# Kernel optimization log

Measured on AMD Instinct MI355X. Metric: run time of the kernel, lower is better.

## Reference

```python
import jax, jax.numpy as jnp
import numpy as np

B, C, H, W = 8, 1, 384, 384
INF2 = float(H * H + W * W + 1)  # 'infinite' squared distance


def _edt_single(feat):
    # Exact Euclidean distance transform: distance from every pixel to the
    # nearest True pixel in `feat` [H, W]. Separable squared-distance min.
    j = jnp.arange(W)
    dj2 = ((j[:, None] - j[None, :]).astype(jnp.float32)) ** 2  # [W, W']
    # g2[i, j] = min_{j': feat[i, j']} (j - j')^2
    g2 = jnp.min(jnp.where(feat[:, None, :], dj2[None, :, :], INF2), axis=2)  # [H, W]
    i = jnp.arange(H)
    di2 = ((i[:, None] - i[None, :]).astype(jnp.float32)) ** 2  # [H, H']
    # d2[i, j] = min_{i'} g2[i', j] + (i - i')^2
    d2 = jnp.min(di2[:, :, None] + g2[None, :, :], axis=1)  # [H, W]
    return jnp.sqrt(jnp.minimum(d2, INF2))


def _distance_map(target):
    # Signed distance map: EDT(1-m) - EDT(m), normalized by global max-abs,
    # matching BoundaryLoss._compute_distance_map (scipy distance_transform_edt).
    m = target.reshape(-1, H, W)

    def per_img(mi):
        fg = mi > 0.5
        pos = _edt_single(fg)        # dist to nearest foreground (EDT of 1-m)
        neg = _edt_single(~fg)       # dist to nearest background (EDT of m)
        return pos - neg

    dist = jax.lax.map(per_img, m).reshape(target.shape)
    maxabs = jnp.max(jnp.abs(dist))
    return jnp.where(maxabs > 0, dist / maxabs, dist)


def _lovasz_flat(logits, labels):
    # Binary Lovasz hinge on flat vectors (one sample).
    signs = 2.0 * labels - 1.0
    errors = 1.0 - logits * signs
    order = jnp.argsort(-errors)          # descending sort, perm is constant w.r.t. grads
    errors_sorted = errors[order]
    gt_sorted = labels[order]
    gts = jnp.sum(gt_sorted)
    intersection = gts - jnp.cumsum(gt_sorted)
    union = gts + jnp.cumsum(1.0 - gt_sorted)
    jaccard = 1.0 - intersection / (union + 1e-7)
    grad = jnp.concatenate([jaccard[:1], jaccard[1:] - jaccard[:-1]])
    return jnp.dot(jax.nn.relu(errors_sorted), grad)


def _combined_loss(pred, target):
    # BCE with logits (stable): max(x,0) - x*z + log1p(exp(-|x|)), mean.
    bce = jnp.mean(jnp.maximum(pred, 0.0) - pred * target + jnp.log1p(jnp.exp(-jnp.abs(pred))))
    # Dice.
    p = jax.nn.sigmoid(pred)
    smooth = 1.0
    intersection = jnp.sum(p * target)
    union = jnp.sum(p) + jnp.sum(target)
    dice = 1.0 - (2.0 * intersection + smooth) / (union + smooth)
    # Boundary: mean(sigmoid(pred) * signed_dist_map(target)); dist map is constant.
    dist_map = jax.lax.stop_gradient(_distance_map(target))
    boundary = jnp.mean(p * dist_map)
    # Lovasz hinge, per-sample over flattened pixels, then mean over batch.
    lovasz = jnp.mean(jax.vmap(_lovasz_flat)(pred.reshape(B, -1), target.reshape(B, -1)))
    loss = 0.3 * bce + 0.3 * dice + 0.2 * boundary + 0.2 * lovasz
    return jnp.clip(loss, 0.0, 100.0)


def setup_inputs() -> dict:
    key = jax.random.key(0)
    k1, k2 = jax.random.split(key)
    pred = jax.random.normal(k1, (B, C, H, W), dtype=jnp.float32)
    target = (jax.random.uniform(k2, (B, C, H, W)) < 0.3).astype(jnp.float32)
    return {"pred": pred, "target": target}


def reference(pred, target):
    return _combined_loss(pred, target)
```

## Files before the change

kernel.cpp:

```cpp
#include <hip/hip_runtime.h>
#include <hip/hip_bf16.h>
#include <math.h>

#define PSZ   147456
#define NTOT  1179648
#define WW    384
#define HH    384
#define NIMG  8
#define NBINH 2048
#define INF2F 294913.0f
#define GV2   1152
#define HPART 8

static __device__ __forceinline__ float errval(float x, float z) {
    float s = __fsub_rn(__fmul_rn(2.0f, z), 1.0f);
    return __fsub_rn(1.0f, __fmul_rn(x, s));
}
static __device__ __forceinline__ int binof(float e) {
    int b = (int)(__fmul_rn(e, 256.0f));
    return b > (NBINH - 1) ? (NBINH - 1) : b;
}
static __device__ __forceinline__ float d2f(int d) {
    return (float)(d * d);
}

struct DPair { int df, db; };
static __device__ __forceinline__ DPair ndist2(const unsigned long long* __restrict__ m, int p) {
    const int BIG = 1 << 20;
    int q = p >> 6, b = p & 63;
    int df = BIG, db = BIG;
    {
        unsigned long long w = m[q];
        unsigned long long tf = w >> b;
        unsigned long long tb = (~w) >> b;
        if (tf) df = __builtin_ctzll(tf);
        if (tb) db = __builtin_ctzll(tb);
        for (int u = q + 1; (df == BIG || db == BIG) && u < 6; ++u) {
            w = m[u];
            if (df == BIG && w)  df = u * 64 + __builtin_ctzll(w)  - p;
            if (db == BIG && ~w) db = u * 64 + __builtin_ctzll(~w) - p;
        }
    }
    {
        unsigned long long w = m[q];
        unsigned long long tf = w << (63 - b);
        unsigned long long tb = (~w) << (63 - b);
        int lf = BIG, lb = BIG;
        if (tf) lf = __builtin_clzll(tf);
        if (tb) lb = __builtin_clzll(tb);
        for (int u = q - 1; (lf == BIG || lb == BIG) && u >= 0; --u) {
            w = m[u];
            if (lf == BIG && w)  lf = p - (u * 64 + 63 - __builtin_clzll(w));
            if (lb == BIG && ~w) lb = p - (u * 64 + 63 - __builtin_clzll(~w));
        }
        if (lf < df) df = lf;
        if (lb < db) db = lb;
    }
    DPair r;
    r.df = (df > 600) ? 600 : df;
    r.db = (db > 600) ? 600 : db;
    return r;
}

__global__ __launch_bounds__(1024) void k_pre(const float* __restrict__ tgt,
                                              const float* __restrict__ pred,
                                              unsigned int* __restrict__ g2,
                                              unsigned long long* __restrict__ histp,
                                              unsigned int* __restrict__ maxabsBits,
                                              unsigned int* __restrict__ elect) {
    __shared__ unsigned long long h[NBINH * 2];
    for (int q = threadIdx.x; q < NBINH * 2; q += 1024) h[q] = 0ull;
    if (blockIdx.x == 0 && threadIdx.x == 0) { maxabsBits[0] = 0u; elect[0] = 0u; }
    __syncthreads();
    int img  = blockIdx.x & 7;
    int part = blockIdx.x >> 3;
    int wv = threadIdx.x >> 6, l = threadIdx.x & 63;
#pragma unroll
    for (int rr = 0; rr < 3; ++rr) {
        int row = img * HH + part * 48 + wv * 3 + rr;
        const float* tr = tgt  + (size_t)row * WW;
        const float* pr = pred + (size_t)row * WW;
        float zv[6], xv[6];
        unsigned long long mf[6];
#pragma unroll
        for (int c = 0; c < 6; ++c) { zv[c] = tr[c * 64 + l]; xv[c] = pr[c * 64 + l]; }
#pragma unroll
        for (int c = 0; c < 6; ++c) mf[c] = __ballot(zv[c] > 0.5f);
        size_t ob = (size_t)row * WW;
#pragma unroll
        for (int c = 0; c < 6; ++c) {
            int p = c * 64 + l;
            DPair d = ndist2(mf, p);
            g2[ob + p] = (unsigned int)d.df | ((unsigned int)d.db << 16);
            float e = errval(xv[c], zv[c]);
            if (e > 0.0f) {
                int lab = (zv[c] > 0.5f) ? 1 : 0;
                unsigned long long add = (1ull << 46) |
                    (unsigned long long)__fmul_rn(e, 16777216.0f);
                atomicAdd(&h[(binof(e) << 1) + lab], add);
            }
        }
    }
    __syncthreads();
    unsigned long long* gh = histp + ((size_t)blockIdx.x << 12);
    for (int q = threadIdx.x; q < NBINH * 2; q += 1024) gh[q] = h[q];
}

__global__ __launch_bounds__(256) void k_fused(const float* __restrict__ pred,
                                               const float* __restrict__ tgt,
                                               const unsigned int* __restrict__ g2,
                                               float* __restrict__ pB, float* __restrict__ pP,
                                               float* __restrict__ pPT, float* __restrict__ pBnd,
                                               unsigned int* __restrict__ pPc,
                                               unsigned int* __restrict__ maxabsBits) {
    int t = threadIdx.x;
    int img = blockIdx.x & 7;
    int bb  = blockIdx.x >> 3;
    int v   = bb * 256 + t;
    int j   = v % WW;
    int i0  = (v / WW) * 4;
    const unsigned int* g2i = g2 + (size_t)img * PSZ;
    unsigned int w[24];
#pragma unroll
    for (int k = 0; k < 24; ++k) {
        int rr = i0 - 8 + k;
        rr = rr < 0 ? 0 : (rr > HH - 1 ? HH - 1 : rr);
        w[k] = g2i[rr * WW + j];
    }
    float aF[4], aB[4];
#pragma unroll
    for (int m = 0; m < 4; ++m) {
        float f = INF2F, g = INF2F;
#pragma unroll
        for (int k = m; k <= m + 16; ++k) {
            float r2 = d2f(k - 8 - m);
            f = fminf(f, r2 + d2f((int)(w[k] & 0xffffu)));
            g = fminf(g, r2 + d2f((int)(w[k] >> 16)));
        }
        aF[m] = f; aB[m] = g;
    }
#pragma unroll
    for (int m = 0; m < 4; ++m) {
        int i = i0 + m;
        for (int r = 9; r < HH; ++r) {
            float r2 = d2f(r);
            if (r2 >= fmaxf(aF[m], aB[m])) break;
            int up = i - r, dn = i + r;
            if (up >= 0) {
                unsigned int ww = g2i[up * WW + j];
                aF[m] = fminf(aF[m], r2 + d2f((int)(ww & 0xffffu)));
                aB[m] = fminf(aB[m], r2 + d2f((int)(ww >> 16)));
            }
            if (dn < HH) {
                unsigned int ww = g2i[dn * WW + j];
                aF[m] = fminf(aF[m], r2 + d2f((int)(ww & 0xffffu)));
                aB[m] = fminf(aB[m], r2 + d2f((int)(ww >> 16)));
            }
        }
    }
    float vals[6] = {0.f, 0.f, 0.f, 0.f, 0.f, 0.f};
#pragma unroll
    for (int m = 0; m < 4; ++m) {
        int n = img * PSZ + (i0 + m) * WW + j;
        float x = pred[n], z = tgt[n];
        bool lab = z > 0.5f;
        float dv = lab ? -sqrtf(fminf(aB[m], INF2F)) : sqrtf(fminf(aF[m], INF2F));
        float bce = fmaxf(x, 0.0f) - x * z + log1pf(expf(-fabsf(x)));
        float p = 1.0f / (1.0f + expf(-x));
        vals[0] += bce; vals[1] += p;
        vals[2] += lab ? p : 0.0f;
        vals[3] += p * dv;
        vals[4] += lab ? 1.0f : 0.0f;
        vals[5] = fmaxf(vals[5], fabsf(dv));
    }
#pragma unroll
    for (int k = 0; k < 5; ++k)
#pragma unroll
        for (int off = 32; off; off >>= 1) vals[k] += __shfl_xor(vals[k], off);
#pragma unroll
    for (int off = 32; off; off >>= 1) vals[5] = fmaxf(vals[5], __shfl_xor(vals[5], off));
    __shared__ float sw[4][6];
    int wv = t >> 6, lnn = t & 63;
    if (lnn == 0) {
#pragma unroll
        for (int k = 0; k < 6; ++k) sw[wv][k] = vals[k];
    }
    __syncthreads();
    if (t < 6) {
        int k = t;
        if (k == 5) {
            float a = fmaxf(fmaxf(sw[0][5], sw[1][5]), fmaxf(sw[2][5], sw[3][5]));
            atomicMax(maxabsBits, __float_as_uint(a));
        } else {
            float a = sw[0][k] + sw[1][k] + sw[2][k] + sw[3][k];
            if (k == 0) pB[blockIdx.x] = a;
            else if (k == 1) pP[blockIdx.x] = a;
            else if (k == 2) pPT[blockIdx.x] = a;
            else if (k == 3) pBnd[blockIdx.x] = a;
            else pPc[blockIdx.x] = (unsigned int)(a + 0.5f);
        }
    }
}

__global__ __launch_bounds__(256) void k_scanlov(const unsigned long long* __restrict__ histp,
                                                 const unsigned int* __restrict__ pPc,
                                                 const float* __restrict__ pB, const float* __restrict__ pP,
                                                 const float* __restrict__ pPT, const float* __restrict__ pBnd,
                                                 double* __restrict__ sums,
                                                 const unsigned int* __restrict__ maxabsBits,
                                                 unsigned int* __restrict__ elect,
                                                 float* __restrict__ out) {
    int b = blockIdx.x, t = threadIdx.x;
    __shared__ double dred[256];
    __shared__ unsigned int ured[256];
    double mv[4] = {0.0, 0.0, 0.0, 0.0};
    unsigned int mc = 0;
    if (t < 144) {
        int q = b + 8 * t;
        mv[0] = (double)pB[q]; mv[1] = (double)pP[q];
        mv[2] = (double)pPT[q]; mv[3] = (double)pBnd[q];
        mc = pPc[q];
    }
    ured[t] = mc; __syncthreads();
    for (int s = 128; s > 0; s >>= 1) { if (t < s) ured[t] += ured[t + s]; __syncthreads(); }
    unsigned int Pfull = ured[0];
    __syncthreads();
#pragma unroll
    for (int a = 0; a < 4; ++a) {
        dred[t] = mv[a]; __syncthreads();
        for (int s = 128; s > 0; s >>= 1) { if (t < s) dred[t] += dred[t + s]; __syncthreads(); }
        if (t == 0) sums[b * 6 + a] = dred[0];
        __syncthreads();
    }
    int m0 = t * 8;
    unsigned int ln = 0, lp = 0;
    unsigned int hcn[8], hcp[8];
    unsigned long long hsn[8], hsp[8];
#pragma unroll
    for (int k = 0; k < 8; ++k) {
        unsigned long long vn = 0ull, vp = 0ull;
#pragma unroll
        for (int pp = 0; pp < HPART; ++pp) {
            const unsigned long long* hc = histp + ((size_t)(pp * 8 + b) << 12);
            vn += hc[2 * (m0 + k)];
            vp += hc[2 * (m0 + k) + 1];
        }
        hcn[k] = (unsigned int)(vn >> 46); hcp[k] = (unsigned int)(vp >> 46);
        hsn[k] = vn & ((1ull << 46) - 1);  hsp[k] = vp & ((1ull << 46) - 1);
        ln += hcn[k]; lp += hcp[k];
    }
    int lane = t & 63, wv = t >> 6;
    unsigned int sln = ln, slp = lp;
#pragma unroll
    for (int off = 1; off < 64; off <<= 1) {
        unsigned int an = __shfl_up(sln, off);
        unsigned int ap = __shfl_up(slp, off);
        if (lane >= off) { sln += an; slp += ap; }
    }
    __shared__ unsigned int wN[4], wP[4];
    if (lane == 63) { wN[wv] = sln; wP[wv] = slp; }
    __syncthreads();
    unsigned int baseN = 0, baseP = 0, totN = 0, totP = 0;
#pragma unroll
    for (int q = 0; q < 4; ++q) {
        if (q < wv) { baseN += wN[q]; baseP += wP[q]; }
        totN += wN[q]; totP += wP[q];
    }
    unsigned int runN = baseN + sln - ln;
    unsigned int runP = baseP + slp - lp;
    const double EPS = 1e-7;
    const double SCL = 1.0 / 16777216.0;
    double P = (double)Pfull;
    double l = 0.0;
#pragma unroll
    for (int k = 0; k < 8; ++k) {
        unsigned int hn = hcn[k], hp = hcp[k];
        if (hn | hp) {
            double negAbove = (double)(totN - runN - hn);
            double D0 = P + negAbove + EPS;
            if (hp) l += ((double)hsp[k] * SCL) / D0;
            if (hn) {
                double pAbove = (double)(totP - runP);
                double D1 = D0 + (double)hn;
                l += (P - pAbove) * ((double)hsn[k] * SCL) / (D0 * D1);
            }
            runN += hn; runP += hp;
        }
    }
    dred[t] = l; __syncthreads();
    for (int s = 128; s > 0; s >>= 1) { if (t < s) dred[t] += dred[t + s]; __syncthreads(); }
    if (t == 0) {
        sums[b * 6 + 4] = dred[0];
        sums[b * 6 + 5] = (double)Pfull;
    }
    __syncthreads();
    __shared__ unsigned int amLast;
    if (t == 0) {
        __threadfence();
        amLast = (atomicAdd(elect, 1u) == NIMG - 1) ? 1u : 0u;
    }
    __syncthreads();
    if (amLast && t == 0) {
        __threadfence();
        double sumBCE = 0, sumP = 0, sumPT = 0, sumBD = 0, sumLV = 0, tsum = 0;
        for (int q = 0; q < NIMG; ++q) {
            sumBCE += sums[q * 6 + 0];
            sumP   += sums[q * 6 + 1];
            sumPT  += sums[q * 6 + 2];
            sumBD  += sums[q * 6 + 3];
            sumLV  += sums[q * 6 + 4];
            tsum   += sums[q * 6 + 5];
        }
        double bce = sumBCE / (double)NTOT;
        double dice = 1.0 - (2.0 * sumPT + 1.0) / (sumP + tsum + 1.0);
        float ma = __uint_as_float(maxabsBits[0]);
        double bnd = sumBD / (double)NTOT;
        if (ma > 0.0f) bnd = bnd / (double)ma;
        double lov = sumLV / (double)NIMG;
        double loss = 0.3 * bce + 0.3 * dice + 0.2 * bnd + 0.2 * lov;
        if (loss < 0.0) loss = 0.0;
        if (loss > 100.0) loss = 100.0;
        out[0] = (float)loss;
    }
}

extern "C" void kernel_launch(void* const* d_in, const int* in_sizes, int n_in,
                              void* d_out, int out_size, void* d_ws, size_t ws_size,
                              hipStream_t stream) {
    const float* pred = (const float*)d_in[0];
    const float* tgt  = (const float*)d_in[1];
    char* ws = (char*)d_ws;

    size_t off = 0;
    unsigned long long* histp = (unsigned long long*)(ws + off);
    off += (size_t)NIMG * HPART * NBINH * 2 * 8;
    unsigned int* maxabsBits = (unsigned int*)(ws + off); off += 64;
    unsigned int* elect      = (unsigned int*)(ws + off); off += 64;
    off = (off + 1023) & ~(size_t)1023;
    double* sums = (double*)(ws + off); off += NIMG * 6 * 8;
    off = (off + 63) & ~(size_t)63;
    float* pB   = (float*)(ws + off); off += (size_t)GV2 * 4;
    float* pP   = (float*)(ws + off); off += (size_t)GV2 * 4;
    float* pPT  = (float*)(ws + off); off += (size_t)GV2 * 4;
    float* pBnd = (float*)(ws + off); off += (size_t)GV2 * 4;
    unsigned int* pPc = (unsigned int*)(ws + off); off += (size_t)GV2 * 4;
    off = (off + 1023) & ~(size_t)1023;
    unsigned int* g2 = (unsigned int*)(ws + off); off += (size_t)NIMG * PSZ * 4;
    (void)off; (void)ws_size; (void)in_sizes; (void)n_in; (void)out_size;

    k_pre<<<NIMG * HPART, 1024, 0, stream>>>(tgt, pred, g2, histp, maxabsBits, elect);
    k_fused<<<GV2, 256, 0, stream>>>(pred, tgt, g2, pB, pP, pPT, pBnd, pPc, maxabsBits);
    k_scanlov<<<NIMG, 256, 0, stream>>>(histp, pPc, pB, pP, pPT, pBnd, sums,
                                        maxabsBits, elect, (float*)d_out);
}
```

Baseline: 54.12 us.

## Split fused pre-pass into separate row-EDT and Lovasz histogram kernels

The single 64-block pre-pass kernel, which computed row-wise nearest-pixel distances and the Lovasz error histogram together, becomes two kernels. The row-EDT kernel uses 768 small blocks of 256 threads, one wave per row. The histogram kernel uses twice as many partitions per image (16) over contiguous pixel chunks. The aim is to spread the pre-pass across far more CUs than the original 64 large blocks could occupy. The cost is an extra kernel launch, a second read of the target tensor, and a larger set of partial histograms to merge in the scan kernel.

```diff
diff --git a/kernel.cpp b/kernel.cpp
--- a/kernel.cpp
+++ b/kernel.cpp
@@ -10,7 +10,9 @@
 #define NBINH 2048
 #define INF2F 294913.0f
 #define GV2   1152
-#define HPART 8
+#define EBLK  768
+#define HPART 16
+#define HPXB  9216
 
 static __device__ __forceinline__ float errval(float x, float z) {
     float s = __fsub_rn(__fmul_rn(2.0f, z), 1.0f);
@@ -62,43 +64,48 @@
     return r;
 }
 
-__global__ __launch_bounds__(1024) void k_pre(const float* __restrict__ tgt,
-                                              const float* __restrict__ pred,
+__global__ __launch_bounds__(256) void k_edth(const float* __restrict__ tgt,
                                               unsigned int* __restrict__ g2,
-                                              unsigned long long* __restrict__ histp,
                                               unsigned int* __restrict__ maxabsBits,
                                               unsigned int* __restrict__ elect) {
+    if (blockIdx.x == 0 && threadIdx.x == 0) { maxabsBits[0] = 0u; elect[0] = 0u; }
+    int img = blockIdx.x & 7;
+    int bb  = blockIdx.x >> 3;
+    int row = img * HH + bb * 4 + (threadIdx.x >> 6);
+    int l = threadIdx.x & 63;
+    const float* tr = tgt + (size_t)row * WW;
+    unsigned long long mf[6];
+#pragma unroll
+    for (int c = 0; c < 6; ++c)
+        mf[c] = __ballot(tr[c * 64 + l] > 0.5f);
+    size_t ob = (size_t)row * WW;
+#pragma unroll
+    for (int c = 0; c < 6; ++c) {
+        int p = c * 64 + l;
+        DPair d = ndist2(mf, p);
+        g2[ob + p] = (unsigned int)d.df | ((unsigned int)d.db << 16);
+    }
+}
+
+__global__ __launch_bounds__(1024) void k_hist(const float* __restrict__ pred,
+                                               const float* __restrict__ tgt,
+                                               unsigned long long* __restrict__ histp) {
     __shared__ unsigned long long h[NBINH * 2];
     for (int q = threadIdx.x; q < NBINH * 2; q += 1024) h[q] = 0ull;
-    if (blockIdx.x == 0 && threadIdx.x == 0) { maxabsBits[0] = 0u; elect[0] = 0u; }
     __syncthreads();
     int img  = blockIdx.x & 7;
     int part = blockIdx.x >> 3;
-    int wv = threadIdx.x >> 6, l = threadIdx.x & 63;
-#pragma unroll
-    for (int rr = 0; rr < 3; ++rr) {
-        int row = img * HH + part * 48 + wv * 3 + rr;
-        const float* tr = tgt  + (size_t)row * WW;
-        const float* pr = pred + (size_t)row * WW;
-        float zv[6], xv[6];
-        unsigned long long mf[6];
-#pragma unroll
-        for (int c = 0; c < 6; ++c) { zv[c] = tr[c * 64 + l]; xv[c] = pr[c * 64 + l]; }
-#pragma unroll
-        for (int c = 0; c < 6; ++c) mf[c] = __ballot(zv[c] > 0.5f);
-        size_t ob = (size_t)row * WW;
-#pragma unroll
-        for (int c = 0; c < 6; ++c) {
-            int p = c * 64 + l;
-            DPair d = ndist2(mf, p);
-            g2[ob + p] = (unsigned int)d.df | ((unsigned int)d.db << 16);
-            float e = errval(xv[c], zv[c]);
-            if (e > 0.0f) {
-                int lab = (zv[c] > 0.5f) ? 1 : 0;
-                unsigned long long add = (1ull << 46) |
-                    (unsigned long long)__fmul_rn(e, 16777216.0f);
-                atomicAdd(&h[(binof(e) << 1) + lab], add);
-            }
+    int base = img * PSZ + part * HPXB;
+#pragma unroll
+    for (int it = 0; it < HPXB / 1024; ++it) {
+        int n = base + it * 1024 + threadIdx.x;
+        float x = pred[n], z = tgt[n];
+        float e = errval(x, z);
+        if (e > 0.0f) {
+            int lab = (z > 0.5f) ? 1 : 0;
+            unsigned long long add = (1ull << 46) |
+                (unsigned long long)__fmul_rn(e, 16777216.0f);
+            atomicAdd(&h[(binof(e) << 1) + lab], add);
         }
     }
     __syncthreads();
@@ -348,7 +355,8 @@
     unsigned int* g2 = (unsigned int*)(ws + off); off += (size_t)NIMG * PSZ * 4;
     (void)off; (void)ws_size; (void)in_sizes; (void)n_in; (void)out_size;
 
-    k_pre<<<NIMG * HPART, 1024, 0, stream>>>(tgt, pred, g2, histp, maxabsBits, elect);
+    k_edth<<<EBLK, 256, 0, stream>>>(tgt, g2, maxabsBits, elect);
+    k_hist<<<NIMG * HPART, 1024, 0, stream>>>(pred, tgt, histp);
     k_fused<<<GV2, 256, 0, stream>>>(pred, tgt, g2, pB, pP, pPT, pBnd, pPc, maxabsBits);
     k_scanlov<<<NIMG, 256, 0, stream>>>(histp, pPc, pB, pP, pPT, pBnd, sums,
                                         maxabsBits, elect, (float*)d_out);
```

Result: slower. 55.64 us (+2.8%).
